# Optimization experiments

Hardware: AMD Instinct MI355X
Metric: run time of the kernel (lower is better)

Reference implementation:

```python
import jax, jax.numpy as jnp
import numpy as np

D_MODEL = 320
N_CH = 129
N_TIMES = 200
D_STATE = 32
HEADDIM = 32
D_CONV = 4
N_LAYERS = 4
N_HEADS = 16
EPS = 1e-5


def _ln(x, w, b):
    m = jnp.mean(x, -1, keepdims=True)
    v = jnp.var(x, -1, keepdims=True)
    return (x - m) / jnp.sqrt(v + EPS) * w + b


def _mha(x, wqkv, bqkv, wo, bo, h):
    # torch nn.MultiheadAttention (batch_first, eval mode, avg attn weights)
    B, L, D = x.shape
    hd = D // h
    qkv = x @ wqkv.T + bqkv
    q, k, v = jnp.split(qkv, 3, axis=-1)
    sp = lambda t: t.reshape(B, L, h, hd).transpose(0, 2, 1, 3)
    q, k, v = sp(q), sp(k), sp(v)
    attn = jax.nn.softmax(jnp.einsum('bhqd,bhkd->bhqk', q, k) / np.sqrt(hd).astype(np.float32), axis=-1)
    o = jnp.einsum('bhqk,bhkd->bhqd', attn, v).transpose(0, 2, 1, 3).reshape(B, L, D)
    return o @ wo.T + bo, attn.mean(axis=1)


def _mamba2(u, in_w, conv_w, conv_b, dt_bias, A_log, Dskip, gn_w, out_w):
    # Mamba2 block, reference (non-fused) path, ngroups=1
    B, L, D = u.shape
    din = 2 * D
    H = din // HEADDIM
    P, N = HEADDIM, D_STATE
    zxbcdt = u @ in_w.T                       # (B,L,2*din+2N+H)
    z = zxbcdt[..., :din]
    xBC = zxbcdt[..., din:2 * din + 2 * N]
    dt = jax.nn.softplus(zxbcdt[..., -H:] + dt_bias)   # (B,L,H)
    # causal depthwise conv1d, kernel D_CONV, then silu
    xp = jnp.pad(xBC, ((0, 0), (D_CONV - 1, 0), (0, 0)))
    xc = conv_b + sum(xp[:, k:k + L, :] * conv_w[:, k] for k in range(D_CONV))
    xc = xc * jax.nn.sigmoid(xc)
    xh = xc[..., :din].reshape(B, L, H, P)
    Bm = xc[..., din:din + N]                 # (B,L,N)
    Cm = xc[..., din + N:]                    # (B,L,N)
    dA = jnp.exp(dt * (-jnp.exp(A_log)))      # (B,L,H)

    def step(st, inp):
        dA_t, dt_t, x_t, B_t, C_t = inp
        st = st * dA_t[:, :, None, None] + jnp.einsum('bh,bhp,bn->bhpn', dt_t, x_t, B_t)
        return st, jnp.einsum('bhpn,bn->bhp', st, C_t)

    mv = lambda t: jnp.moveaxis(t, 1, 0)
    st0 = jnp.zeros((B, H, P, N), u.dtype)
    _, ys = jax.lax.scan(step, st0, (mv(dA), mv(dt), mv(xh), mv(Bm), mv(Cm)))
    y = jnp.moveaxis(ys, 0, 1) + Dskip[None, None, :, None] * xh   # (B,L,H,P)
    y = y.reshape(B, L, din) * (z * jax.nn.sigmoid(z))             # gate
    y = y * jax.lax.rsqrt(jnp.mean(y * y, -1, keepdims=True) + EPS) * gn_w
    return y @ out_w.T


def _forward(x, sp_conv_w, sp_conv_b, sp_qkv_w, sp_qkv_b, sp_out_w, sp_out_b,
             sp_ln1_w, sp_ln1_b, sp_ff1_w, sp_ff1_b, sp_ff2_w, sp_ff2_b,
             sp_ln2_w, sp_ln2_b, norm_in_w, norm_in_b,
             m_in_w, m_conv_w, m_conv_b, m_dt_bias, m_A_log, m_D, m_gnorm_w, m_out_w,
             ln_w, ln_b, pm_qkv_w, pm_qkv_b, pm_out_w, pm_out_b, pm_ln_w, pm_ln_b,
             pool_w1, pool_b1, pool_w2, pool_b2, head_w1, head_b1, head_w2, head_b2):
    # spatial encoder: 1x1 conv projection -> MHA -> FFN
    h = jnp.einsum('bcl,dc->bld', x, sp_conv_w) + sp_conv_b        # (B,L,D)
    ha, sp_attn = _mha(h, sp_qkv_w, sp_qkv_b, sp_out_w, sp_out_b, N_HEADS)
    h = _ln(h + ha, sp_ln1_w, sp_ln1_b)
    ff = jax.nn.gelu(h @ sp_ff1_w.T + sp_ff1_b, approximate=False) @ sp_ff2_w.T + sp_ff2_b
    h = _ln(h + ff, sp_ln2_w, sp_ln2_b)
    h = _ln(h, norm_in_w, norm_in_b)
    # stacked pre-norm Mamba2 blocks with residuals
    for i in range(N_LAYERS):
        res = h
        h = _ln(h, ln_w[i], ln_b[i])
        h = _mamba2(h, m_in_w[i], m_conv_w[i], m_conv_b[i], m_dt_bias[i],
                    m_A_log[i], m_D[i], m_gnorm_w[i], m_out_w[i])
        h = h + res
    ha, post_attn = _mha(h, pm_qkv_w, pm_qkv_b, pm_out_w, pm_out_b, N_HEADS)
    h = _ln(h + ha, pm_ln_w, pm_ln_b)
    # attention-weighted pooling
    a = jnp.tanh(h @ pool_w1.T + pool_b1) @ pool_w2.T + pool_b2    # (B,L,1)
    a = jax.nn.softmax(a, axis=1)
    pooled = jnp.sum(h * a, axis=1)                                # (B,D)
    hr = jax.nn.gelu(pooled @ head_w1.T + head_b1, approximate=False)
    out = hr @ head_w2.T + head_b2                                 # (B,1)
    return out, sp_attn, post_attn, a.squeeze(-1)


def setup_inputs() -> dict:
    key = jax.random.key(0)
    ks = iter(jax.random.split(key, 64))
    nrm = lambda shape, s=0.02: jax.random.normal(next(ks), shape, jnp.float32) * s
    d, C, L, B = D_MODEL, N_CH, N_TIMES, 128
    din = 2 * d
    Hm = din // HEADDIM                       # 20 SSM heads
    dproj = 2 * din + 2 * D_STATE + Hm        # 1364
    cdim = din + 2 * D_STATE                  # 704
    nl = N_LAYERS
    return {
        'x': jax.random.normal(next(ks), (B, C, L), jnp.float32),
        'sp_conv_w': nrm((d, C)), 'sp_conv_b': jnp.zeros((d,), jnp.float32),
        'sp_qkv_w': nrm((3 * d, d)), 'sp_qkv_b': jnp.zeros((3 * d,), jnp.float32),
        'sp_out_w': nrm((d, d)), 'sp_out_b': jnp.zeros((d,), jnp.float32),
        'sp_ln1_w': jnp.ones((d,), jnp.float32), 'sp_ln1_b': jnp.zeros((d,), jnp.float32),
        'sp_ff1_w': nrm((2 * d, d)), 'sp_ff1_b': jnp.zeros((2 * d,), jnp.float32),
        'sp_ff2_w': nrm((d, 2 * d)), 'sp_ff2_b': jnp.zeros((d,), jnp.float32),
        'sp_ln2_w': jnp.ones((d,), jnp.float32), 'sp_ln2_b': jnp.zeros((d,), jnp.float32),
        'norm_in_w': jnp.ones((d,), jnp.float32), 'norm_in_b': jnp.zeros((d,), jnp.float32),
        'm_in_w': nrm((nl, dproj, d)),
        'm_conv_w': nrm((nl, cdim, D_CONV), 0.2),
        'm_conv_b': jnp.zeros((nl, cdim), jnp.float32),
        'm_dt_bias': jax.random.uniform(next(ks), (nl, Hm), jnp.float32, -0.1, 0.1),
        'm_A_log': jnp.log(jax.random.uniform(next(ks), (nl, Hm), jnp.float32, 1.0, 16.0)),
        'm_D': jnp.ones((nl, Hm), jnp.float32),
        'm_gnorm_w': jnp.ones((nl, din), jnp.float32),
        'm_out_w': nrm((nl, d, din)),
        'ln_w': jnp.ones((nl, d), jnp.float32), 'ln_b': jnp.zeros((nl, d), jnp.float32),
        'pm_qkv_w': nrm((3 * d, d)), 'pm_qkv_b': jnp.zeros((3 * d,), jnp.float32),
        'pm_out_w': nrm((d, d)), 'pm_out_b': jnp.zeros((d,), jnp.float32),
        'pm_ln_w': jnp.ones((d,), jnp.float32), 'pm_ln_b': jnp.zeros((d,), jnp.float32),
        'pool_w1': nrm((d // 4, d)), 'pool_b1': jnp.zeros((d // 4,), jnp.float32),
        'pool_w2': nrm((1, d // 4)), 'pool_b2': jnp.zeros((1,), jnp.float32),
        'head_w1': nrm((d // 2, d)), 'head_b1': jnp.zeros((d // 2,), jnp.float32),
        'head_w2': nrm((1, d // 2)), 'head_b2': jnp.zeros((1,), jnp.float32),
    }


def reference(x, sp_conv_w, sp_conv_b, sp_qkv_w, sp_qkv_b, sp_out_w, sp_out_b,
              sp_ln1_w, sp_ln1_b, sp_ff1_w, sp_ff1_b, sp_ff2_w, sp_ff2_b,
              sp_ln2_w, sp_ln2_b, norm_in_w, norm_in_b,
              m_in_w, m_conv_w, m_conv_b, m_dt_bias, m_A_log, m_D, m_gnorm_w, m_out_w,
              ln_w, ln_b, pm_qkv_w, pm_qkv_b, pm_out_w, pm_out_b, pm_ln_w, pm_ln_b,
              pool_w1, pool_b1, pool_w2, pool_b2, head_w1, head_b1, head_w2, head_b2):
    return _forward(x, sp_conv_w, sp_conv_b, sp_qkv_w, sp_qkv_b, sp_out_w, sp_out_b,
                    sp_ln1_w, sp_ln1_b, sp_ff1_w, sp_ff1_b, sp_ff2_w, sp_ff2_b,
                    sp_ln2_w, sp_ln2_b, norm_in_w, norm_in_b,
                    m_in_w, m_conv_w, m_conv_b, m_dt_bias, m_A_log, m_D, m_gnorm_w, m_out_w,
                    ln_w, ln_b, pm_qkv_w, pm_qkv_b, pm_out_w, pm_out_b, pm_ln_w, pm_ln_b,
                    pool_w1, pool_b1, pool_w2, pool_b2, head_w1, head_b1, head_w2, head_b2)
```

## Files before the change

kernel.cpp:

```cpp
#include <hip/hip_runtime.h>
#include <math.h>

#define BB 128
#define LL 200
#define DM 320
#define RTOT (BB*LL)
#define NCH 129
#define DIN 640
#define HM 20
#define PP 32
#define NN 32
#define CDIM 704
#define DPROJ 1364
#define NH 16
#define HD 20
#define ATTN_SCALE 0.22360679774997896f

#define CH 32
#define NCHUNK 4
#define RC (CH*LL)

static __device__ __forceinline__ float sigmoidf_(float x){ return 1.f/(1.f+__expf(-x)); }
static __device__ __forceinline__ float geluf_(float x){ return 0.5f*x*(1.f+erff(x*0.70710678118654752f)); }

__global__ __launch_bounds__(256) void k_transpose(const float* __restrict__ x, float* __restrict__ xT){
  int idx = blockIdx.x*256 + threadIdx.x;
  if (idx >= BB*LL*NCH) return;
  int r = idx / NCH, c = idx - r*NCH;
  int b = r / LL, l = r - b*LL;
  xT[idx] = x[((size_t)b*NCH + c)*LL + l];
}

#define BM 128
#define BN 64
#define BKK 16
__global__ __launch_bounds__(256) void k_gemm(const float* __restrict__ A, const float* __restrict__ W,
    const float* __restrict__ bias, float* __restrict__ C, int M, int N, int K, int act, int accum){
  __shared__ float As[BKK][BM+4];
  __shared__ float Ws[BKK][BN+4];
  int tid = threadIdx.x;
  int m0 = blockIdx.y*BM, n0 = blockIdx.x*BN;
  int tx = tid & 15, ty = tid >> 4;
  float acc[8][4];
  #pragma unroll
  for (int i=0;i<8;i++)
    #pragma unroll
    for (int j=0;j<4;j++) acc[i][j]=0.f;
  bool kvec = ((K & 3) == 0);
  for (int k0 = 0; k0 < K; k0 += BKK) {
    if (kvec) {
      int r = tid >> 2, c4 = (tid & 3) << 2;
      #pragma unroll
      for (int hfl = 0; hfl < 2; hfl++) {
        int rr = r + hfl*64;
        float4 v = make_float4(0.f,0.f,0.f,0.f);
        if (m0 + rr < M && k0 + c4 < K)
          v = *(const float4*)(A + (size_t)(m0+rr)*K + k0 + c4);
        As[c4+0][rr]=v.x; As[c4+1][rr]=v.y; As[c4+2][rr]=v.z; As[c4+3][rr]=v.w;
      }
      {
        int n = tid >> 2;
        float4 v = make_float4(0.f,0.f,0.f,0.f);
        if (n0 + n < N && k0 + c4 < K)
          v = *(const float4*)(W + (size_t)(n0+n)*K + k0 + c4);
        Ws[c4+0][n]=v.x; Ws[c4+1][n]=v.y; Ws[c4+2][n]=v.z; Ws[c4+3][n]=v.w;
      }
    } else {
      #pragma unroll
      for (int e = 0; e < 8; e++) {
        int lin = e*256 + tid;
        int r = lin >> 4, c = lin & 15;
        float v = 0.f;
        if (m0 + r < M && k0 + c < K) v = A[(size_t)(m0+r)*K + k0 + c];
        As[c][r] = v;
      }
      #pragma unroll
      for (int e = 0; e < 4; e++) {
        int lin = e*256 + tid;
        int n = lin >> 4, c = lin & 15;
        float v = 0.f;
        if (n0 + n < N && k0 + c < K) v = W[(size_t)(n0+n)*K + k0 + c];
        Ws[c][n] = v;
      }
    }
    __syncthreads();
    #pragma unroll
    for (int kk = 0; kk < BKK; kk++) {
      float af[8], bf[4];
      float4 a0 = *(const float4*)&As[kk][ty*8];
      float4 a1 = *(const float4*)&As[kk][ty*8+4];
      af[0]=a0.x; af[1]=a0.y; af[2]=a0.z; af[3]=a0.w;
      af[4]=a1.x; af[5]=a1.y; af[6]=a1.z; af[7]=a1.w;
      float4 b0 = *(const float4*)&Ws[kk][tx*4];
      bf[0]=b0.x; bf[1]=b0.y; bf[2]=b0.z; bf[3]=b0.w;
      #pragma unroll
      for (int i=0;i<8;i++)
        #pragma unroll
        for (int j=0;j<4;j++) acc[i][j] = fmaf(af[i], bf[j], acc[i][j]);
// ... 7 lines not shown
    #pragma unroll
    for (int j=0;j<4;j++){
      int n = n0 + tx*4 + j;
      if (n >= N) continue;
      float v = acc[i][j];
      if (bias) v += bias[n];
      if (act == 1) v = geluf_(v);
      else if (act == 2) v = tanhf(v);
      size_t off = (size_t)m*N + n;
      if (accum) v += C[off];
      C[off] = v;
    }
  }
}

__global__ __launch_bounds__(256) void k_ln(const float* __restrict__ A, const float* __restrict__ Badd,
    float* __restrict__ O, const float* __restrict__ w, const float* __restrict__ b, int nrows){
  int wid = threadIdx.x >> 6, lane = threadIdx.x & 63;
  int row = blockIdx.x*4 + wid;
  if (row >= nrows) return;
  const float* a = A + (size_t)row*DM;
  float x[5]; float s = 0.f;
  #pragma unroll
  for (int j=0;j<5;j++){
    int c = lane + j*64;
    x[j] = a[c];
    if (Badd) x[j] += Badd[(size_t)row*DM + c];
    s += x[j];
  }
  #pragma unroll
  for (int m=1;m<64;m<<=1) s += __shfl_xor(s, m);
  float mean = s * (1.f/DM);
  float vs = 0.f;
  #pragma unroll
  for (int j=0;j<5;j++){ float d = x[j]-mean; vs += d*d; }
  #pragma unroll
  for (int m=1;m<64;m<<=1) vs += __shfl_xor(vs, m);
  float inv = rsqrtf(vs*(1.f/DM) + 1e-5f);
  float* o = O + (size_t)row*DM;
  #pragma unroll
  for (int j=0;j<5;j++){
    int c = lane + j*64;
    o[c] = (x[j]-mean)*inv*w[c] + b[c];
  }
}

__global__ __launch_bounds__(256) void k_attn1(const float* __restrict__ qkv,
    float* __restrict__ oout, float* __restrict__ ml){
  __shared__ float Ks[LL*HD];
  __shared__ float Vs[LL*HD];
  int b = blockIdx.x >> 4, h = blockIdx.x & 15;
  int tid = threadIdx.x;
  for (int idx = tid; idx < LL*HD; idx += 256) {
    int r = idx / HD, c = idx - r*HD;
    const float* base = qkv + (size_t)(b*LL+r)*960 + h*HD + c;
    Ks[idx] = base[320];
    Vs[idx] = base[640];
  }
  __syncthreads();
  int q = tid;
  if (q >= LL) return;
  const float* qp = qkv + (size_t)(b*LL+q)*960 + h*HD;
  float qr[HD];
// ... 8 lines not shown
  for (int d=0; d<HD; d++) o[d]=0.f;
  for (int k = 0; k < LL; k++) {
    float s = 0.f;
    #pragma unroll
    for (int d = 0; d < HD; d++) s = fmaf(qr[d], Ks[k*HD+d], s);
    s *= ATTN_SCALE;
    float nm = fmaxf(m, s);
    float al = __expf(m - nm);
    float p  = __expf(s - nm);
    l = l*al + p;
    #pragma unroll
    for (int d = 0; d < HD; d++) o[d] = fmaf(p, Vs[k*HD+d], o[d]*al);
    m = nm;
  }
  float inv = 1.f/l;
  float* op = oout + (size_t)(b*LL+q)*DM + h*HD;
  #pragma unroll
  for (int d = 0; d < HD; d++) op[d] = o[d]*inv;
  size_t mlb = ((size_t)(b*NH+h)*LL + q)*2;
  ml[mlb+0] = m;
  ml[mlb+1] = l;
}

#define QS 164
__global__ __launch_bounds__(256) void k_attnmean(const float* __restrict__ qkv,
    const float* __restrict__ ml, float* __restrict__ outp){
  __shared__ float Qs[32*QS];
  __shared__ float Ksh[32*QS];
  __shared__ float Ms[NH*32];
  __shared__ float Ls[NH*32];
  int b = blockIdx.z;
  int q0 = blockIdx.y*32, k0 = blockIdx.x*32;
  int tid = threadIdx.x;
// ... 37 lines not shown
          float4 v = *(const float4*)&Qs[qr*QS + hh*HD + d4*4];
          s += v.x*kf[d4*4] + v.y*kf[d4*4+1] + v.z*kf[d4*4+2] + v.w*kf[d4*4+3];
        }
        acc[j] += __expf(s*ATTN_SCALE - Ms[h*32 + qr]) * Ls[h*32 + qr];
      }
    }
  }
  #pragma unroll
  for (int j = 0; j < 4; j++) {
    int q = q0 + ty + j*8, k = k0 + tx;
    if (q < LL && k < LL)
      outp[(size_t)(b*LL+q)*LL + k] = acc[j] * (1.f/NH);
  }
}

__global__ __launch_bounds__(256) void k_dtdA(const float* __restrict__ big, const float* __restrict__ dtb,
    const float* __restrict__ alog, float* __restrict__ dt, float* __restrict__ da, int nrows){
  int idx = blockIdx.x*256 + threadIdx.x;
  if (idx >= nrows*HM) return;
  int row = idx / HM, h = idx - row*HM;
  float raw = big[(size_t)row*DPROJ + 1344 + h] + dtb[h];
  float sp = (raw > 30.f) ? raw : log1pf(__expf(raw));
  dt[idx] = sp;
  da[idx] = __expf(-__expf(alog[h]) * sp);
}

__global__ __launch_bounds__(256) void k_conv(const float* __restrict__ big, const float* __restrict__ cw,
    const float* __restrict__ cb, float* __restrict__ xc, int nrows){
  int idx = blockIdx.x*256 + threadIdx.x;
  if (idx >= nrows*CDIM) return;
  int row = idx / CDIM, c = idx - row*CDIM;
  int l = row % LL;
  float acc = cb[c];
  #pragma unroll
  for (int k = 0; k < 4; k++) {
    int li = l - 3 + k;
    if (li >= 0) acc = fmaf(big[(size_t)(row-3+k)*DPROJ + 640 + c], cw[c*4+k], acc);
  }
  xc[idx] = acc * sigmoidf_(acc);
}

__global__ __launch_bounds__(256) void k_scan(const float* __restrict__ xc, const float* __restrict__ dt,
    const float* __restrict__ da, float* __restrict__ y){
  __shared__ float xs[LL*PP];
  __shared__ float dts[LL];
  __shared__ float das[LL];
  int b = blockIdx.x / HM, h = blockIdx.x - (blockIdx.x/HM)*HM;
  int tid = threadIdx.x;
  for (int idx = tid; idx < LL*PP; idx += 256) {
    int r = idx >> 5, c = idx & 31;
    xs[idx] = xc[(size_t)(b*LL+r)*CDIM + h*PP + c];
  }
  for (int idx = tid; idx < LL; idx += 256) {
    dts[idx] = dt[(b*LL+idx)*HM + h];
    das[idx] = da[(b*LL+idx)*HM + h];
  }
  __syncthreads();
  int p = tid >> 3, ng = tid & 7, n0 = ng*4;
  float st0=0.f, st1=0.f, st2=0.f, st3=0.f;
  const float* base = xc + (size_t)(b*LL)*CDIM;
  float4 Bc = *(const float4*)(base + 640 + n0);
  float4 Cc = *(const float4*)(base + 672 + n0);
  for (int t = 0; t < LL; t++) {
    float4 Bn = Bc, Cn = Cc;
    if (t < LL-1) {
      Bn = *(const float4*)(base + (size_t)(t+1)*CDIM + 640 + n0);
      Cn = *(const float4*)(base + (size_t)(t+1)*CDIM + 672 + n0);
    }
    float dav = das[t], dtv = dts[t];
    float coef = dtv * xs[t*PP + p];
    st0 = fmaf(coef, Bc.x, st0*dav);
    st1 = fmaf(coef, Bc.y, st1*dav);
    st2 = fmaf(coef, Bc.z, st2*dav);
    st3 = fmaf(coef, Bc.w, st3*dav);
    float part = st0*Cc.x + st1*Cc.y + st2*Cc.z + st3*Cc.w;
    part += __shfl_xor(part, 1);
    part += __shfl_xor(part, 2);
    part += __shfl_xor(part, 4);
    if (ng == 0) y[(size_t)(b*LL+t)*DIN + h*PP + p] = part;
    Bc = Bn; Cc = Cn;
  }
}

__global__ __launch_bounds__(256) void k_mpost(float* __restrict__ y, const float* __restrict__ xc,
    const float* __restrict__ zbuf, const float* __restrict__ Dp, const float* __restrict__ gw, int nrows){
  int wid = threadIdx.x >> 6, lane = threadIdx.x & 63;
  int row = blockIdx.x*4 + wid;
  if (row >= nrows) return;
  float v[10]; float ss = 0.f;
  #pragma unroll
  for (int j = 0; j < 10; j++) {
    int c = lane + j*64;
    float ys = y[(size_t)row*DIN + c];
    float xh = xc[(size_t)row*CDIM + c];
    float z  = zbuf[(size_t)row*DPROJ + c];
    float val = (ys + Dp[c>>5]*xh) * (z * sigmoidf_(z));
    v[j] = val; ss += val*val;
  }
  #pragma unroll
  for (int m=1;m<64;m<<=1) ss += __shfl_xor(ss, m);
  float scale = rsqrtf(ss*(1.f/DIN) + 1e-5f);
  #pragma unroll
  for (int j = 0; j < 10; j++) {
    int c = lane + j*64;
    y[(size_t)row*DIN + c] = v[j]*scale*gw[c];
  }
}

__global__ __launch_bounds__(256) void k_pool2(const float* __restrict__ A, const float* __restrict__ w2,
    const float* __restrict__ b2, float* __restrict__ out, int nrows){
  int row = blockIdx.x*256 + threadIdx.x;
  if (row >= nrows) return;
  float s = b2[0];
  const float* a = A + (size_t)row*80;
  #pragma unroll
  for (int j = 0; j < 80; j++) s = fmaf(a[j], w2[j], s);
  out[row] = s;
}

__global__ __launch_bounds__(256) void k_pool(const float* __restrict__ logits, const float* __restrict__ h,
// ... 17 lines not shown
    pooled[b*DM + d] = s;
  }
}

__global__ __launch_bounds__(128) void k_head2(const float* __restrict__ hr, const float* __restrict__ w2,
    const float* __restrict__ b2, float* __restrict__ out){
  int b = threadIdx.x;
  if (b >= BB) return;
  float s = b2[0];
  const float* a = hr + (size_t)b*160;
  #pragma unroll
  for (int j = 0; j < 160; j++) s = fmaf(a[j], w2[j], s);
  out[b] = s;
}

static inline void gemm_launch(const float* A, const float* W, const float* bias, float* C,
    int M, int N, int K, int act, int accum, hipStream_t s){
  dim3 g((N+BN-1)/BN, (M+BM-1)/BM);
  hipLaunchKernelGGL(k_gemm, g, dim3(256), 0, s, A, W, bias, C, M, N, K, act, accum);
}

#define F_H    ((size_t)0)
#define F_T    ((size_t)8192000)
#define F_S    ((size_t)16384000)
#define F_BIGC ((size_t)16384000)
#define F_XCC  ((size_t)25113600)
#define F_YC   ((size_t)29619200)
#define F_DTC  ((size_t)33715200)
#define F_DAC  ((size_t)33843200)
#define F_QKVC ((size_t)16384000)
#define F_MLC  ((size_t)22528000)
#define F_DEST ((size_t)22732800)
#define F_FF1  ((size_t)16384000)
#define F_XT   ((size_t)16384000)
#define F_P1   ((size_t)16384000)
#define F_LOG  ((size_t)18432000)
#define F_PL   ((size_t)18457600)
#define F_HR   ((size_t)18498560)

#define O_OUT ((size_t)0)
#define O_A1  ((size_t)128)
#define O_A2  ((size_t)5120128)
#define O_A   ((size_t)10240128)

extern "C" void kernel_launch(void* const* d_in, const int* in_sizes, int n_in,
                              void* d_out, int out_size, void* d_ws, size_t ws_size,
                              hipStream_t stream) {
  const float* x         = (const float*)d_in[0];
  const float* sp_conv_w = (const float*)d_in[1];
  const float* sp_conv_b = (const float*)d_in[2];
  const float* sp_qkv_w  = (const float*)d_in[3];
  const float* sp_qkv_b  = (const float*)d_in[4];
  const float* sp_out_w  = (const float*)d_in[5];
// ... 23 lines not shown
  const float* pm_out_w  = (const float*)d_in[29];
  const float* pm_out_b  = (const float*)d_in[30];
  const float* pm_ln_w   = (const float*)d_in[31];
  const float* pm_ln_b   = (const float*)d_in[32];
  const float* pool_w1   = (const float*)d_in[33];
  const float* pool_b1   = (const float*)d_in[34];
  const float* pool_w2   = (const float*)d_in[35];
  const float* pool_b2   = (const float*)d_in[36];
  const float* head_w1   = (const float*)d_in[37];
  const float* head_b1   = (const float*)d_in[38];
  const float* head_w2   = (const float*)d_in[39];
  const float* head_b2   = (const float*)d_in[40];

  float* ws  = (float*)d_ws;
  float* H   = ws + F_H;
  float* T   = ws + F_T;
  float* out = (float*)d_out;

  hipLaunchKernelGGL(k_transpose, dim3((BB*LL*NCH+255)/256), dim3(256), 0, stream, x, ws + F_XT);
  gemm_launch(ws + F_XT, sp_conv_w, sp_conv_b, H, RTOT, DM, NCH, 0, 0, stream);

  for (int c = 0; c < NCHUNK; c++) {
    const float* Hc = H + (size_t)c*RC*DM;
    gemm_launch(Hc, sp_qkv_w, sp_qkv_b, ws + F_QKVC, RC, 3*DM, DM, 0, 0, stream);
    hipLaunchKernelGGL(k_attn1, dim3(CH*NH), dim3(256), 0, stream, ws + F_QKVC,
                       T + (size_t)c*RC*DM, ws + F_MLC);
    hipLaunchKernelGGL(k_attnmean, dim3(7,7,CH), dim3(256), 0, stream, ws + F_QKVC,
                       ws + F_MLC, out + O_A1 + (size_t)c*RC*LL);
  }
  gemm_launch(T, sp_out_w, sp_out_b, ws + F_DEST, RTOT, DM, DM, 0, 0, stream);
  hipLaunchKernelGGL(k_ln, dim3(RTOT/4), dim3(256), 0, stream, H, ws + F_DEST, H, sp_ln1_w, sp_ln1_b, RTOT);

  gemm_launch(H, sp_ff1_w, sp_ff1_b, ws + F_FF1, RTOT, DIN, DM, 1, 0, stream);
  gemm_launch(ws + F_FF1, sp_ff2_w, sp_ff2_b, T, RTOT, DM, DIN, 0, 0, stream);
  hipLaunchKernelGGL(k_ln, dim3(RTOT/4), dim3(256), 0, stream, H, T, H, sp_ln2_w, sp_ln2_b, RTOT);
  hipLaunchKernelGGL(k_ln, dim3(RTOT/4), dim3(256), 0, stream, H, (const float*)nullptr, H, norm_in_w, norm_in_b, RTOT);

  for (int i = 0; i < 4; i++) {
    hipLaunchKernelGGL(k_ln, dim3(RTOT/4), dim3(256), 0, stream, H, (const float*)nullptr, T,
                       ln_w + (size_t)i*DM, ln_b + (size_t)i*DM, RTOT);
    for (int c = 0; c < NCHUNK; c++) {
      const float* Tc = T + (size_t)c*RC*DM;
      float* BIGc = ws + F_BIGC;
      float* XCc  = ws + F_XCC;
      float* Yc   = ws + F_YC;
      float* DTc  = ws + F_DTC;
      float* DAc  = ws + F_DAC;
      gemm_launch(Tc, m_in_w + (size_t)i*DPROJ*DM, nullptr, BIGc, RC, DPROJ, DM, 0, 0, stream);
      hipLaunchKernelGGL(k_dtdA, dim3((RC*HM+255)/256), dim3(256), 0, stream, BIGc,
                         m_dt_bias + (size_t)i*HM, m_A_log + (size_t)i*HM, DTc, DAc, RC);
      hipLaunchKernelGGL(k_conv, dim3((RC*CDIM+255)/256), dim3(256), 0, stream, BIGc,
                         m_conv_w + (size_t)i*CDIM*4, m_conv_b + (size_t)i*CDIM, XCc, RC);
      hipLaunchKernelGGL(k_scan, dim3(CH*HM), dim3(256), 0, stream, XCc, DTc, DAc, Yc);
      hipLaunchKernelGGL(k_mpost, dim3(RC/4), dim3(256), 0, stream, Yc, XCc, BIGc,
                         m_D + (size_t)i*HM, m_gnorm_w + (size_t)i*DIN, RC);
      gemm_launch(Yc, m_out_w + (size_t)i*DM*DIN, nullptr, H + (size_t)c*RC*DM, RC, DM, DIN, 0, 1, stream);
    }
  }

  for (int c = 0; c < NCHUNK; c++) {
    const float* Hc = H + (size_t)c*RC*DM;
    gemm_launch(Hc, pm_qkv_w, pm_qkv_b, ws + F_QKVC, RC, 3*DM, DM, 0, 0, stream);
    hipLaunchKernelGGL(k_attn1, dim3(CH*NH), dim3(256), 0, stream, ws + F_QKVC,
                       T + (size_t)c*RC*DM, ws + F_MLC);
    hipLaunchKernelGGL(k_attnmean, dim3(7,7,CH), dim3(256), 0, stream, ws + F_QKVC,
                       ws + F_MLC, out + O_A2 + (size_t)c*RC*LL);
  }
  gemm_launch(T, pm_out_w, pm_out_b, ws + F_DEST, RTOT, DM, DM, 0, 0, stream);
  hipLaunchKernelGGL(k_ln, dim3(RTOT/4), dim3(256), 0, stream, H, ws + F_DEST, H, pm_ln_w, pm_ln_b, RTOT);

  gemm_launch(H, pool_w1, pool_b1, ws + F_P1, RTOT, 80, DM, 2, 0, stream);
  hipLaunchKernelGGL(k_pool2, dim3((RTOT+255)/256), dim3(256), 0, stream, ws + F_P1, pool_w2, pool_b2, ws + F_LOG, RTOT);
  hipLaunchKernelGGL(k_pool, dim3(BB), dim3(256), 0, stream, ws + F_LOG, H, out + O_A, ws + F_PL);
  gemm_launch(ws + F_PL, head_w1, head_b1, ws + F_HR, BB, 160, DM, 1, 0, stream);
  hipLaunchKernelGGL(k_head2, dim3(1), dim3(128), 0, stream, ws + F_HR, head_w2, head_b2, out + O_OUT);
}
```

Before: 7.652 ms.

## Replace FP32 SIMT GEMMs with split-bf16 MFMA GEMMs and restructure chunked pipeline

Swaps the scalar FP32 tiled GEMM for an MFMA bf16 kernel. Each FP32 operand is split into three bf16 parts (hi/mid/lo) and six cross products are accumulated to keep near-FP32 accuracy. Producers (LN, attention, mpost, transpose) now emit the split bf16 triples directly, and weights are split on every call. It also fuses the double LayerNorm, folds dt/dA into the scan, and re-chunks the spatial and Mamba stages. The aim is to use matrix cores for the GEMM-bound work, at the cost of six MFMAs per product, extra split traffic and per-call weight-splitting kernels.

```diff
diff --git a/kernel.cpp b/kernel.cpp
--- a/kernel.cpp
+++ b/kernel.cpp
@@ -15,20 +15,123 @@
 #define NH 16
 #define HD 20
 #define ATTN_SCALE 0.22360679774997896f
+#define KCONV 160
 
 #define CH 32
 #define NCHUNK 4
 #define RC (CH*LL)
+#define CHB 16
+#define NCHUNKB 8
+#define RCB (CHB*LL)
+
+typedef unsigned short ushort;
+typedef __attribute__((ext_vector_type(8))) short v8s;
+typedef __attribute__((ext_vector_type(4))) float v4f;
 
 static __device__ __forceinline__ float sigmoidf_(float x){ return 1.f/(1.f+__expf(-x)); }
 static __device__ __forceinline__ float geluf_(float x){ return 0.5f*x*(1.f+erff(x*0.70710678118654752f)); }
-
-__global__ __launch_bounds__(256) void k_transpose(const float* __restrict__ x, float* __restrict__ xT){
-  int idx = blockIdx.x*256 + threadIdx.x;
-  if (idx >= BB*LL*NCH) return;
-  int r = idx / NCH, c = idx - r*NCH;
-  int b = r / LL, l = r - b*LL;
-  xT[idx] = x[((size_t)b*NCH + c)*LL + l];
+static __device__ __forceinline__ ushort f2bf(float f){
+  unsigned u = __float_as_uint(f);
+  u = (u + 0x7FFFu + ((u>>16)&1u)) >> 16;
+  return (ushort)u;
+}
+static __device__ __forceinline__ float bf2f(ushort h){ return __uint_as_float(((unsigned)h)<<16); }
+static __device__ __forceinline__ void split3(float v, ushort* h, ushort* m, ushort* l){
+  ushort hh = f2bf(v);
+  float r1 = v - bf2f(hh);
+  ushort mm = f2bf(r1);
+  float r2 = r1 - bf2f(mm);
+  *h = hh; *m = mm; *l = f2bf(r2);
+}
+
+__global__ __launch_bounds__(256) void k_mgemm(
+    const ushort* __restrict__ AH, const ushort* __restrict__ AM, const ushort* __restrict__ AL,
+    const ushort* __restrict__ WH, const ushort* __restrict__ WM, const ushort* __restrict__ WL,
+    const float* __restrict__ bias,
+    float* __restrict__ outF, ushort* __restrict__ outH, ushort* __restrict__ outM, ushort* __restrict__ outL,
+    int M, int N, int K, int act, int accum){
+  __shared__ ushort sA[3][128*32];
+  __shared__ ushort sW[3][128*32];
+  int tid = threadIdx.x;
+  int wid = tid>>6, lane = tid&63;
+  int quad = lane>>4, col = lane&15;
+  int m0 = blockIdx.y*128, n0 = blockIdx.x*128;
+  int wm = (wid&1)*64, wn = (wid>>1)*64;
+  v4f acc[4][4];
+  #pragma unroll
+  for (int i=0;i<4;i++)
+    #pragma unroll
+    for (int j=0;j<4;j++) acc[i][j] = (v4f)(0.f);
+
+  int r0 = tid>>2, kc0 = (tid&3)<<3;
+  int r1 = r0 + 64, kc1 = kc0;
+  int wrow0 = n0+r0; if (wrow0 > N-1) wrow0 = N-1;
+  int wrow1 = n0+r1; if (wrow1 > N-1) wrow1 = N-1;
+  const ushort* pA[3] = {AH, AM, AL};
+  const ushort* pW[3] = {WH, WM, WL};
+  size_t aoff0 = (size_t)(m0+r0)*K + kc0;
+  size_t aoff1 = (size_t)(m0+r1)*K + kc1;
+  size_t woff0 = (size_t)wrow0*K + kc0;
+  size_t woff1 = (size_t)wrow1*K + kc1;
+  int so0 = r0*32 + kc0, so1 = r1*32 + kc1;
+
+  for (int kb = 0; kb < K; kb += 32) {
+    #pragma unroll
+    for (int s=0;s<3;s++){
+      v8s va0 = *(const v8s*)(pA[s]+aoff0+kb);
+      v8s va1 = *(const v8s*)(pA[s]+aoff1+kb);
+      v8s vw0 = *(const v8s*)(pW[s]+woff0+kb);
+      v8s vw1 = *(const v8s*)(pW[s]+woff1+kb);
+      *(v8s*)&sA[s][so0]=va0; *(v8s*)&sA[s][so1]=va1;
+      *(v8s*)&sW[s][so0]=vw0; *(v8s*)&sW[s][so1]=vw1;
+    }
+    __syncthreads();
+    v8s af[3][4];
+    #pragma unroll
+    for (int i=0;i<4;i++){
+      int ro = (wm+16*i+col)*32 + quad*8;
+      af[0][i] = *(const v8s*)&sA[0][ro];
+      af[1][i] = *(const v8s*)&sA[1][ro];
+      af[2][i] = *(const v8s*)&sA[2][ro];
+    }
+    #pragma unroll
+    for (int j=0;j<4;j++){
+      int ro = (wn+16*j+col)*32 + quad*8;
+      v8s b0 = *(const v8s*)&sW[0][ro];
+      v8s b1 = *(const v8s*)&sW[1][ro];
+      v8s b2 = *(const v8s*)&sW[2][ro];
+      #pragma unroll
+      for (int i=0;i<4;i++){
+        acc[i][j] = __builtin_amdgcn_mfma_f32_16x16x32_bf16(af[2][i], b0, acc[i][j], 0,0,0);
+        acc[i][j] = __builtin_amdgcn_mfma_f32_16x16x32_bf16(af[1][i], b1, acc[i][j], 0,0,0);
+        acc[i][j] = __builtin_amdgcn_mfma_f32_16x16x32_bf16(af[0][i], b2, acc[i][j], 0,0,0);
+        acc[i][j] = __builtin_amdgcn_mfma_f32_16x16x32_bf16(af[1][i], b0, acc[i][j], 0,0,0);
+        acc[i][j] = __builtin_amdgcn_mfma_f32_16x16x32_bf16(af[0][i], b1, acc[i][j], 0,0,0);
+        acc[i][j] = __builtin_amdgcn_mfma_f32_16x16x32_bf16(af[0][i], b0, acc[i][j], 0,0,0);
+      }
+    }
+    __syncthreads();
+  }
+  #pragma unroll
+  for (int i=0;i<4;i++){
+    int mb = m0 + wm + 16*i + quad*4;
+    #pragma unroll
+    for (int j=0;j<4;j++){
+      int n = n0 + wn + 16*j + col;
+      if (n >= N) continue;
+      float bv = bias ? bias[n] : 0.f;
+      #pragma unroll
+      for (int r=0;r<4;r++){
+        float v = acc[i][j][r] + bv;
+        if (act == 1) v = geluf_(v);
+        else if (act == 2) v = tanhf(v);
+        size_t off = (size_t)(mb+r)*N + n;
+        if (accum) v += outF[off];
+        if (outF) outF[off] = v;
+        if (outH) split3(v, outH+off, outM+off, outL+off);
+      }
+    }
+  }
 }
 
 #define BM 128
@@ -46,42 +149,22 @@
   for (int i=0;i<8;i++)
     #pragma unroll
     for (int j=0;j<4;j++) acc[i][j]=0.f;
-  bool kvec = ((K & 3) == 0);
   for (int k0 = 0; k0 < K; k0 += BKK) {
-    if (kvec) {
-      int r = tid >> 2, c4 = (tid & 3) << 2;
-      #pragma unroll
-      for (int hfl = 0; hfl < 2; hfl++) {
-        int rr = r + hfl*64;
-        float4 v = make_float4(0.f,0.f,0.f,0.f);
-        if (m0 + rr < M && k0 + c4 < K)
-          v = *(const float4*)(A + (size_t)(m0+rr)*K + k0 + c4);
-        As[c4+0][rr]=v.x; As[c4+1][rr]=v.y; As[c4+2][rr]=v.z; As[c4+3][rr]=v.w;
-      }
-      {
-        int n = tid >> 2;
-        float4 v = make_float4(0.f,0.f,0.f,0.f);
-        if (n0 + n < N && k0 + c4 < K)
-          v = *(const float4*)(W + (size_t)(n0+n)*K + k0 + c4);
-        Ws[c4+0][n]=v.x; Ws[c4+1][n]=v.y; Ws[c4+2][n]=v.z; Ws[c4+3][n]=v.w;
-      }
-    } else {
-      #pragma unroll
-      for (int e = 0; e < 8; e++) {
-        int lin = e*256 + tid;
-        int r = lin >> 4, c = lin & 15;
-        float v = 0.f;
-        if (m0 + r < M && k0 + c < K) v = A[(size_t)(m0+r)*K + k0 + c];
-        As[c][r] = v;
-      }
-      #pragma unroll
-      for (int e = 0; e < 4; e++) {
-        int lin = e*256 + tid;
-        int n = lin >> 4, c = lin & 15;
-        float v = 0.f;
-        if (n0 + n < N && k0 + c < K) v = W[(size_t)(n0+n)*K + k0 + c];
-        Ws[c][n] = v;
-      }
+    int r = tid >> 2, c4 = (tid & 3) << 2;
+    #pragma unroll
+    for (int hfl = 0; hfl < 2; hfl++) {
+      int rr = r + hfl*64;
+      float4 v = make_float4(0.f,0.f,0.f,0.f);
+      if (m0 + rr < M && k0 + c4 < K)
+        v = *(const float4*)(A + (size_t)(m0+rr)*K + k0 + c4);
+      As[c4+0][rr]=v.x; As[c4+1][rr]=v.y; As[c4+2][rr]=v.z; As[c4+3][rr]=v.w;
+    }
+    {
+      int n = tid >> 2;
+      float4 v = make_float4(0.f,0.f,0.f,0.f);
+      if (n0 + n < N && k0 + c4 < K)
+        v = *(const float4*)(W + (size_t)(n0+n)*K + k0 + c4);
+      Ws[c4+0][n]=v.x; Ws[c4+1][n]=v.y; Ws[c4+2][n]=v.z; Ws[c4+3][n]=v.w;
     }
     __syncthreads();
     #pragma unroll
@@ -119,8 +202,36 @@
   }
 }
 
+__global__ __launch_bounds__(256) void k_wsplit(const float* __restrict__ src, ushort* __restrict__ hi,
+    ushort* __restrict__ mi, ushort* __restrict__ lo, int N, int K, int Kp){
+  int idx = blockIdx.x*256 + threadIdx.x;
+  if (idx >= N*Kp) return;
+  int n = idx / Kp, k = idx - n*Kp;
+  float v = (k < K) ? src[(size_t)n*K + k] : 0.f;
+  split3(v, hi+idx, mi+idx, lo+idx);
+}
+
+__global__ __launch_bounds__(256) void k_split(const float* __restrict__ src, ushort* __restrict__ hi,
+    ushort* __restrict__ mi, ushort* __restrict__ lo, int n){
+  int idx = blockIdx.x*256 + threadIdx.x;
+  if (idx >= n) return;
+  split3(src[idx], hi+idx, mi+idx, lo+idx);
+}
+
+__global__ __launch_bounds__(256) void k_tsplit(const float* __restrict__ x, ushort* __restrict__ hi,
+    ushort* __restrict__ mi, ushort* __restrict__ lo, int r0g){
+  int idx = blockIdx.x*256 + threadIdx.x;
+  if (idx >= RC*KCONV) return;
+  int r = idx / KCONV, c = idx - r*KCONV;
+  int gr = r0g + r;
+  int b = gr / LL, l = gr - b*LL;
+  float v = (c < NCH) ? x[((size_t)b*NCH + c)*LL + l] : 0.f;
+  split3(v, hi+idx, mi+idx, lo+idx);
+}
+
 __global__ __launch_bounds__(256) void k_ln(const float* __restrict__ A, const float* __restrict__ Badd,
-    float* __restrict__ O, const float* __restrict__ w, const float* __restrict__ b, int nrows){
+    float* __restrict__ Of, ushort* __restrict__ Oh, ushort* __restrict__ Om, ushort* __restrict__ Ol,
+    const float* __restrict__ w, const float* __restrict__ b, int nrows){
   int wid = threadIdx.x >> 6, lane = threadIdx.x & 63;
   int row = blockIdx.x*4 + wid;
   if (row >= nrows) return;
@@ -142,16 +253,64 @@
   #pragma unroll
   for (int m=1;m<64;m<<=1) vs += __shfl_xor(vs, m);
   float inv = rsqrtf(vs*(1.f/DM) + 1e-5f);
-  float* o = O + (size_t)row*DM;
   #pragma unroll
   for (int j=0;j<5;j++){
     int c = lane + j*64;
-    o[c] = (x[j]-mean)*inv*w[c] + b[c];
+    float v = (x[j]-mean)*inv*w[c] + b[c];
+    size_t off = (size_t)row*DM + c;
+    if (Of) Of[off] = v;
+    if (Oh) split3(v, Oh+off, Om+off, Ol+off);
+  }
+}
+
+__global__ __launch_bounds__(256) void k_ln2x(const float* __restrict__ A, const float* __restrict__ F,
+    const float* __restrict__ w2, const float* __restrict__ b2,
+    const float* __restrict__ w3, const float* __restrict__ b3,
+    float* __restrict__ O, int nrows){
+  int wid = threadIdx.x >> 6, lane = threadIdx.x & 63;
+  int row = blockIdx.x*4 + wid;
+  if (row >= nrows) return;
+  float x[5]; float s = 0.f;
+  #pragma unroll
+  for (int j=0;j<5;j++){
+    int c = lane + j*64;
+    x[j] = A[(size_t)row*DM + c] + F[(size_t)row*DM + c];
+    s += x[j];
+  }
+  #pragma unroll
+  for (int m=1;m<64;m<<=1) s += __shfl_xor(s, m);
+  float mean = s * (1.f/DM);
+  float vs = 0.f;
+  #pragma unroll
+  for (int j=0;j<5;j++){ float d = x[j]-mean; vs += d*d; }
+  #pragma unroll
+  for (int m=1;m<64;m<<=1) vs += __shfl_xor(vs, m);
+  float inv = rsqrtf(vs*(1.f/DM) + 1e-5f);
+  float s2 = 0.f;
+  #pragma unroll
+  for (int j=0;j<5;j++){
+    int c = lane + j*64;
+    x[j] = (x[j]-mean)*inv*w2[c] + b2[c];
+    s2 += x[j];
+  }
+  #pragma unroll
+  for (int m=1;m<64;m<<=1) s2 += __shfl_xor(s2, m);
+  float mean2 = s2 * (1.f/DM);
+  float vs2 = 0.f;
+  #pragma unroll
+  for (int j=0;j<5;j++){ float d = x[j]-mean2; vs2 += d*d; }
+  #pragma unroll
+  for (int m=1;m<64;m<<=1) vs2 += __shfl_xor(vs2, m);
+  float inv2 = rsqrtf(vs2*(1.f/DM) + 1e-5f);
+  #pragma unroll
+  for (int j=0;j<5;j++){
+    int c = lane + j*64;
+    O[(size_t)row*DM + c] = (x[j]-mean2)*inv2*w3[c] + b3[c];
   }
 }
 
 __global__ __launch_bounds__(256) void k_attn1(const float* __restrict__ qkv,
-    float* __restrict__ oout, float* __restrict__ ml){
+    ushort* __restrict__ oh, ushort* __restrict__ om, ushort* __restrict__ ol, float* __restrict__ ml){
   __shared__ float Ks[LL*HD];
   __shared__ float Vs[LL*HD];
   int b = blockIdx.x >> 4, h = blockIdx.x & 15;
@@ -190,9 +349,11 @@
     m = nm;
   }
   float inv = 1.f/l;
-  float* op = oout + (size_t)(b*LL+q)*DM + h*HD;
-  #pragma unroll
-  for (int d = 0; d < HD; d++) op[d] = o[d]*inv;
+  size_t ob = (size_t)(b*LL+q)*DM + h*HD;
+  #pragma unroll
+  for (int d = 0; d < HD; d++) {
+    split3(o[d]*inv, oh+ob+d, om+ob+d, ol+ob+d);
+  }
   size_t mlb = ((size_t)(b*NH+h)*LL + q)*2;
   ml[mlb+0] = m;
   ml[mlb+1] = l;
@@ -260,17 +421,6 @@
   }
 }
 
-__global__ __launch_bounds__(256) void k_dtdA(const float* __restrict__ big, const float* __restrict__ dtb,
-    const float* __restrict__ alog, float* __restrict__ dt, float* __restrict__ da, int nrows){
-  int idx = blockIdx.x*256 + threadIdx.x;
-  if (idx >= nrows*HM) return;
-  int row = idx / HM, h = idx - row*HM;
-  float raw = big[(size_t)row*DPROJ + 1344 + h] + dtb[h];
-  float sp = (raw > 30.f) ? raw : log1pf(__expf(raw));
-  dt[idx] = sp;
-  da[idx] = __expf(-__expf(alog[h]) * sp);
-}
-
 __global__ __launch_bounds__(256) void k_conv(const float* __restrict__ big, const float* __restrict__ cw,
     const float* __restrict__ cb, float* __restrict__ xc, int nrows){
   int idx = blockIdx.x*256 + threadIdx.x;
@@ -286,8 +436,8 @@
   xc[idx] = acc * sigmoidf_(acc);
 }
 
-__global__ __launch_bounds__(256) void k_scan(const float* __restrict__ xc, const float* __restrict__ dt,
-    const float* __restrict__ da, float* __restrict__ y){
+__global__ __launch_bounds__(256) void k_scan(const float* __restrict__ xc, const float* __restrict__ big,
+    const float* __restrict__ dtb, const float* __restrict__ alog, float* __restrict__ y){
   __shared__ float xs[LL*PP];
   __shared__ float dts[LL];
   __shared__ float das[LL];
@@ -297,9 +447,13 @@
     int r = idx >> 5, c = idx & 31;
     xs[idx] = xc[(size_t)(b*LL+r)*CDIM + h*PP + c];
   }
+  float aexp = __expf(alog[h]);
+  float dtbh = dtb[h];
   for (int idx = tid; idx < LL; idx += 256) {
-    dts[idx] = dt[(b*LL+idx)*HM + h];
-    das[idx] = da[(b*LL+idx)*HM + h];
+    float raw = big[(size_t)(b*LL+idx)*DPROJ + 1344 + h] + dtbh;
+    float sp = (raw > 30.f) ? raw : log1pf(__expf(raw));
+    dts[idx] = sp;
+    das[idx] = __expf(-aexp * sp);
   }
   __syncthreads();
   int p = tid >> 3, ng = tid & 7, n0 = ng*4;
@@ -328,8 +482,9 @@
   }
 }
 
-__global__ __launch_bounds__(256) void k_mpost(float* __restrict__ y, const float* __restrict__ xc,
-    const float* __restrict__ zbuf, const float* __restrict__ Dp, const float* __restrict__ gw, int nrows){
+__global__ __launch_bounds__(256) void k_mpost(const float* __restrict__ y, const float* __restrict__ xc,
+    const float* __restrict__ zbuf, const float* __restrict__ Dp, const float* __restrict__ gw,
+    ushort* __restrict__ yh, ushort* __restrict__ ym, ushort* __restrict__ yl, int nrows){
   int wid = threadIdx.x >> 6, lane = threadIdx.x & 63;
   int row = blockIdx.x*4 + wid;
   if (row >= nrows) return;
@@ -349,7 +504,9 @@
   #pragma unroll
   for (int j = 0; j < 10; j++) {
     int c = lane + j*64;
-    y[(size_t)row*DIN + c] = v[j]*scale*gw[c];
+    float val = v[j]*scale*gw[c];
+    size_t off = (size_t)row*DIN + c;
+    split3(val, yh+off, ym+off, yl+off);
   }
 }
 
@@ -397,29 +554,77 @@
   out[b] = s;
 }
 
-static inline void gemm_launch(const float* A, const float* W, const float* bias, float* C,
+static inline void mgemm(const ushort* AH, const ushort* AM, const ushort* AL,
+    const ushort* WH, const ushort* WM, const ushort* WL,
+    const float* bias, float* outF, ushort* outH, ushort* outM, ushort* outL,
     int M, int N, int K, int act, int accum, hipStream_t s){
-  dim3 g((N+BN-1)/BN, (M+BM-1)/BM);
-  hipLaunchKernelGGL(k_gemm, g, dim3(256), 0, s, A, W, bias, C, M, N, K, act, accum);
-}
-
-#define F_H    ((size_t)0)
-#define F_T    ((size_t)8192000)
-#define F_S    ((size_t)16384000)
-#define F_BIGC ((size_t)16384000)
-#define F_XCC  ((size_t)25113600)
-#define F_YC   ((size_t)29619200)
-#define F_DTC  ((size_t)33715200)
-#define F_DAC  ((size_t)33843200)
-#define F_QKVC ((size_t)16384000)
-#define F_MLC  ((size_t)22528000)
-#define F_DEST ((size_t)22732800)
-#define F_FF1  ((size_t)16384000)
-#define F_XT   ((size_t)16384000)
-#define F_P1   ((size_t)16384000)
-#define F_LOG  ((size_t)18432000)
-#define F_PL   ((size_t)18457600)
-#define F_HR   ((size_t)18498560)
+  hipLaunchKernelGGL(k_mgemm, dim3((N+127)/128, M/128), dim3(256), 0, s,
+                     AH, AM, AL, WH, WM, WL, bias, outF, outH, outM, outL, M, N, K, act, accum);
+}
+static inline void wsplit(const float* src, ushort* hi, ushort* mi, ushort* lo, int N, int K, int Kp, hipStream_t s){
+  hipLaunchKernelGGL(k_wsplit, dim3((N*Kp+255)/256), dim3(256), 0, s, src, hi, mi, lo, N, K, Kp);
+}
+
+#define F_H      ((size_t)0)
+#define F_WCONVH ((size_t)8192000)
+#define F_WCONVM ((size_t)8217600)
+#define F_WCONVL ((size_t)8243200)
+#define F_WQKVH  ((size_t)8268800)
+#define F_WQKVM  ((size_t)8422400)
+#define F_WQKVL  ((size_t)8576000)
+#define F_WOUTH  ((size_t)8729600)
+#define F_WOUTM  ((size_t)8780800)
+#define F_WOUTL  ((size_t)8832000)
+#define F_WFF1H  ((size_t)8883200)
+#define F_WFF1M  ((size_t)8985600)
+#define F_WFF1L  ((size_t)9088000)
+#define F_WFF2H  ((size_t)9190400)
+#define F_WFF2M  ((size_t)9292800)
+#define F_WFF2L  ((size_t)9395200)
+#define F_WINH   ((size_t)9497600)
+#define F_WINM   ((size_t)10370560)
+#define F_WINL   ((size_t)11243520)
+#define F_WMOH   ((size_t)12116480)
+#define F_WMOM   ((size_t)12526080)
+#define F_WMOL   ((size_t)12935680)
+#define F_WPQH   ((size_t)13345280)
+#define F_WPQM   ((size_t)13498880)
+#define F_WPQL   ((size_t)13652480)
+#define F_WPOH   ((size_t)13806080)
+#define F_WPOM   ((size_t)13857280)
+#define F_WPOL   ((size_t)13908480)
+#define F_WPLH   ((size_t)13959680)
+#define F_WPLM   ((size_t)13972480)
+#define F_WPLL   ((size_t)13985280)
+#define SB       ((size_t)13998080)
+#define S_XTH  (SB+0)
+#define S_XTM  (SB+512000)
+#define S_XTL  (SB+1024000)
+#define S_HH   (SB+1536000)
+#define S_HM   (SB+2560000)
+#define S_HL   (SB+3584000)
+#define S_TH   (SB+4608000)
+#define S_TM   (SB+5632000)
+#define S_TL   (SB+6656000)
+#define S_QKV  (SB+7680000)
+#define S_FF1H (SB+7680000)
+#define S_FF1M (SB+9728000)
+#define S_FF1L (SB+11776000)
+#define S_P1   (SB+7680000)
+#define S_ML   (SB+13824000)
+#define S_DEST (SB+14028800)
+#define S_LOG  (SB+16076800)
+#define S_PL   (SB+16102400)
+#define S_HR   (SB+16143360)
+#define S_MTH  (SB+0)
+#define S_MTM  (SB+512000)
+#define S_MTL  (SB+1024000)
+#define S_BIG  (SB+1536000)
+#define S_XC   (SB+5900800)
+#define S_YC   (SB+8153600)
+#define S_YH   (SB+10201600)
+#define S_YM   (SB+11225600)
+#define S_YL   (SB+12249600)
 
 #define O_OUT ((size_t)0)
 #define O_A1  ((size_t)128)
@@ -473,64 +678,97 @@
 
   float* ws  = (float*)d_ws;
   float* H   = ws + F_H;
-  float* T   = ws + F_T;
   float* out = (float*)d_out;
 
-  hipLaunchKernelGGL(k_transpose, dim3((BB*LL*NCH+255)/256), dim3(256), 0, stream, x, ws + F_XT);
-  gemm_launch(ws + F_XT, sp_conv_w, sp_conv_b, H, RTOT, DM, NCH, 0, 0, stream);
+  #define U(off) ((ushort*)(ws + (off)))
+
+  wsplit(sp_conv_w, U(F_WCONVH), U(F_WCONVM), U(F_WCONVL), DM, NCH, KCONV, stream);
+  wsplit(sp_qkv_w,  U(F_WQKVH),  U(F_WQKVM),  U(F_WQKVL),  3*DM, DM, DM, stream);
+  wsplit(sp_out_w,  U(F_WOUTH),  U(F_WOUTM),  U(F_WOUTL),  DM, DM, DM, stream);
+  wsplit(sp_ff1_w,  U(F_WFF1H),  U(F_WFF1M),  U(F_WFF1L),  DIN, DM, DM, stream);
+  wsplit(sp_ff2_w,  U(F_WFF2H),  U(F_WFF2M),  U(F_WFF2L),  DM, DIN, DIN, stream);
+  for (int i = 0; i < 4; i++) {
+    size_t wo = (size_t)i*DPROJ*DM;
+    wsplit(m_in_w + wo, U(F_WINH)+wo, U(F_WINM)+wo, U(F_WINL)+wo, DPROJ, DM, DM, stream);
+    size_t wo2 = (size_t)i*DM*DIN;
+    wsplit(m_out_w + wo2, U(F_WMOH)+wo2, U(F_WMOM)+wo2, U(F_WMOL)+wo2, DM, DIN, DIN, stream);
+  }
+  wsplit(pm_qkv_w, U(F_WPQH), U(F_WPQM), U(F_WPQL), 3*DM, DM, DM, stream);
+  wsplit(pm_out_w, U(F_WPOH), U(F_WPOM), U(F_WPOL), DM, DM, DM, stream);
+  wsplit(pool_w1,  U(F_WPLH), U(F_WPLM), U(F_WPLL), 80, DM, DM, stream);
 
   for (int c = 0; c < NCHUNK; c++) {
-    const float* Hc = H + (size_t)c*RC*DM;
-    gemm_launch(Hc, sp_qkv_w, sp_qkv_b, ws + F_QKVC, RC, 3*DM, DM, 0, 0, stream);
-    hipLaunchKernelGGL(k_attn1, dim3(CH*NH), dim3(256), 0, stream, ws + F_QKVC,
-                       T + (size_t)c*RC*DM, ws + F_MLC);
-    hipLaunchKernelGGL(k_attnmean, dim3(7,7,CH), dim3(256), 0, stream, ws + F_QKVC,
-                       ws + F_MLC, out + O_A1 + (size_t)c*RC*LL);
-  }
-  gemm_launch(T, sp_out_w, sp_out_b, ws + F_DEST, RTOT, DM, DM, 0, 0, stream);
-  hipLaunchKernelGGL(k_ln, dim3(RTOT/4), dim3(256), 0, stream, H, ws + F_DEST, H, sp_ln1_w, sp_ln1_b, RTOT);
-
-  gemm_launch(H, sp_ff1_w, sp_ff1_b, ws + F_FF1, RTOT, DIN, DM, 1, 0, stream);
-  gemm_launch(ws + F_FF1, sp_ff2_w, sp_ff2_b, T, RTOT, DM, DIN, 0, 0, stream);
-  hipLaunchKernelGGL(k_ln, dim3(RTOT/4), dim3(256), 0, stream, H, T, H, sp_ln2_w, sp_ln2_b, RTOT);
-  hipLaunchKernelGGL(k_ln, dim3(RTOT/4), dim3(256), 0, stream, H, (const float*)nullptr, H, norm_in_w, norm_in_b, RTOT);
+    float* Hc = H + (size_t)c*RC*DM;
+    hipLaunchKernelGGL(k_tsplit, dim3((RC*KCONV+255)/256), dim3(256), 0, stream, x,
+                       U(S_XTH), U(S_XTM), U(S_XTL), c*RC);
+    mgemm(U(S_XTH), U(S_XTM), U(S_XTL), U(F_WCONVH), U(F_WCONVM), U(F_WCONVL), sp_conv_b,
+          Hc, U(S_HH), U(S_HM), U(S_HL), RC, DM, KCONV, 0, 0, stream);
+    mgemm(U(S_HH), U(S_HM), U(S_HL), U(F_WQKVH), U(F_WQKVM), U(F_WQKVL), sp_qkv_b,
+          ws + S_QKV, nullptr, nullptr, nullptr, RC, 3*DM, DM, 0, 0, stream);
+    hipLaunchKernelGGL(k_attn1, dim3(CH*NH), dim3(256), 0, stream, ws + S_QKV,
+                       U(S_TH), U(S_TM), U(S_TL), ws + S_ML);
+    hipLaunchKernelGGL(k_attnmean, dim3(7,7,CH), dim3(256), 0, stream, ws + S_QKV,
+                       ws + S_ML, out + O_A1 + (size_t)c*RC*LL);
+    mgemm(U(S_TH), U(S_TM), U(S_TL), U(F_WOUTH), U(F_WOUTM), U(F_WOUTL), sp_out_b,
+          ws + S_DEST, nullptr, nullptr, nullptr, RC, DM, DM, 0, 0, stream);
+    hipLaunchKernelGGL(k_ln, dim3(RC/4), dim3(256), 0, stream, Hc, ws + S_DEST,
+                       Hc, U(S_HH), U(S_HM), U(S_HL), sp_ln1_w, sp_ln1_b, RC);
+    mgemm(U(S_HH), U(S_HM), U(S_HL), U(F_WFF1H), U(F_WFF1M), U(F_WFF1L), sp_ff1_b,
+          nullptr, U(S_FF1H), U(S_FF1M), U(S_FF1L), RC, DIN, DM, 1, 0, stream);
+    mgemm(U(S_FF1H), U(S_FF1M), U(S_FF1L), U(F_WFF2H), U(F_WFF2M), U(F_WFF2L), sp_ff2_b,
+          ws + S_DEST, nullptr, nullptr, nullptr, RC, DM, DIN, 0, 0, stream);
+    hipLaunchKernelGGL(k_ln2x, dim3(RC/4), dim3(256), 0, stream, Hc, ws + S_DEST,
+                       sp_ln2_w, sp_ln2_b, norm_in_w, norm_in_b, Hc, RC);
+  }
 
   for (int i = 0; i < 4; i++) {
-    hipLaunchKernelGGL(k_ln, dim3(RTOT/4), dim3(256), 0, stream, H, (const float*)nullptr, T,
-                       ln_w + (size_t)i*DM, ln_b + (size_t)i*DM, RTOT);
-    for (int c = 0; c < NCHUNK; c++) {
-      const float* Tc = T + (size_t)c*RC*DM;
-      float* BIGc = ws + F_BIGC;
-      float* XCc  = ws + F_XCC;
-      float* Yc   = ws + F_YC;
-      float* DTc  = ws + F_DTC;
-      float* DAc  = ws + F_DAC;
-      gemm_launch(Tc, m_in_w + (size_t)i*DPROJ*DM, nullptr, BIGc, RC, DPROJ, DM, 0, 0, stream);
-      hipLaunchKernelGGL(k_dtdA, dim3((RC*HM+255)/256), dim3(256), 0, stream, BIGc,
-                         m_dt_bias + (size_t)i*HM, m_A_log + (size_t)i*HM, DTc, DAc, RC);
-      hipLaunchKernelGGL(k_conv, dim3((RC*CDIM+255)/256), dim3(256), 0, stream, BIGc,
-                         m_conv_w + (size_t)i*CDIM*4, m_conv_b + (size_t)i*CDIM, XCc, RC);
-      hipLaunchKernelGGL(k_scan, dim3(CH*HM), dim3(256), 0, stream, XCc, DTc, DAc, Yc);
-      hipLaunchKernelGGL(k_mpost, dim3(RC/4), dim3(256), 0, stream, Yc, XCc, BIGc,
-                         m_D + (size_t)i*HM, m_gnorm_w + (size_t)i*DIN, RC);
-      gemm_launch(Yc, m_out_w + (size_t)i*DM*DIN, nullptr, H + (size_t)c*RC*DM, RC, DM, DIN, 0, 1, stream);
+    const ushort* WIH = U(F_WINH) + (size_t)i*DPROJ*DM;
+    const ushort* WIM = U(F_WINM) + (size_t)i*DPROJ*DM;
+    const ushort* WIL = U(F_WINL) + (size_t)i*DPROJ*DM;
+    const ushort* WOH = U(F_WMOH) + (size_t)i*DM*DIN;
+    const ushort* WOM = U(F_WMOM) + (size_t)i*DM*DIN;
+    const ushort* WOL = U(F_WMOL) + (size_t)i*DM*DIN;
+    for (int c = 0; c < NCHUNKB; c++) {
+      float* Hc = H + (size_t)c*RCB*DM;
+      hipLaunchKernelGGL(k_ln, dim3(RCB/4), dim3(256), 0, stream, Hc, (const float*)nullptr,
+                         (float*)nullptr, U(S_MTH), U(S_MTM), U(S_MTL),
+                         ln_w + (size_t)i*DM, ln_b + (size_t)i*DM, RCB);
+      mgemm(U(S_MTH), U(S_MTM), U(S_MTL), WIH, WIM, WIL, nullptr,
+            ws + S_BIG, nullptr, nullptr, nullptr, RCB, DPROJ, DM, 0, 0, stream);
+      hipLaunchKernelGGL(k_conv, dim3((RCB*CDIM+255)/256), dim3(256), 0, stream, ws + S_BIG,
+                         m_conv_w + (size_t)i*CDIM*4, m_conv_b + (size_t)i*CDIM, ws + S_XC, RCB);
+      hipLaunchKernelGGL(k_scan, dim3(CHB*HM), dim3(256), 0, stream, ws + S_XC, ws + S_BIG,
+                         m_dt_bias + (size_t)i*HM, m_A_log + (size_t)i*HM, ws + S_YC);
+      hipLaunchKernelGGL(k_mpost, dim3(RCB/4), dim3(256), 0, stream, ws + S_YC, ws + S_XC, ws + S_BIG,
+                         m_D + (size_t)i*HM, m_gnorm_w + (size_t)i*DIN,
+                         U(S_YH), U(S_YM), U(S_YL), RCB);
+      mgemm(U(S_YH), U(S_YM), U(S_YL), WOH, WOM, WOL, nullptr,
+            Hc, nullptr, nullptr, nullptr, RCB, DM, DIN, 0, 1, stream);
     }
   }
 
   for (int c = 0; c < NCHUNK; c++) {
-    const float* Hc = H + (size_t)c*RC*DM;
-    gemm_launch(Hc, pm_qkv_w, pm_qkv_b, ws + F_QKVC, RC, 3*DM, DM, 0, 0, stream);
-    hipLaunchKernelGGL(k_attn1, dim3(CH*NH), dim3(256), 0, stream, ws + F_QKVC,
-                       T + (size_t)c*RC*DM, ws + F_MLC);
-    hipLaunchKernelGGL(k_attnmean, dim3(7,7,CH), dim3(256), 0, stream, ws + F_QKVC,
-                       ws + F_MLC, out + O_A2 + (size_t)c*RC*LL);
-  }
-  gemm_launch(T, pm_out_w, pm_out_b, ws + F_DEST, RTOT, DM, DM, 0, 0, stream);
-  hipLaunchKernelGGL(k_ln, dim3(RTOT/4), dim3(256), 0, stream, H, ws + F_DEST, H, pm_ln_w, pm_ln_b, RTOT);
-
-  gemm_launch(H, pool_w1, pool_b1, ws + F_P1, RTOT, 80, DM, 2, 0, stream);
-  hipLaunchKernelGGL(k_pool2, dim3((RTOT+255)/256), dim3(256), 0, stream, ws + F_P1, pool_w2, pool_b2, ws + F_LOG, RTOT);
-  hipLaunchKernelGGL(k_pool, dim3(BB), dim3(256), 0, stream, ws + F_LOG, H, out + O_A, ws + F_PL);
-  gemm_launch(ws + F_PL, head_w1, head_b1, ws + F_HR, BB, 160, DM, 1, 0, stream);
-  hipLaunchKernelGGL(k_head2, dim3(1), dim3(128), 0, stream, ws + F_HR, head_w2, head_b2, out + O_OUT);
-}
+    float* Hc = H + (size_t)c*RC*DM;
+    hipLaunchKernelGGL(k_split, dim3((RC*DM+255)/256), dim3(256), 0, stream, Hc,
+                       U(S_HH), U(S_HM), U(S_HL), RC*DM);
+    mgemm(U(S_HH), U(S_HM), U(S_HL), U(F_WPQH), U(F_WPQM), U(F_WPQL), pm_qkv_b,
+          ws + S_QKV, nullptr, nullptr, nullptr, RC, 3*DM, DM, 0, 0, stream);
+    hipLaunchKernelGGL(k_attn1, dim3(CH*NH), dim3(256), 0, stream, ws + S_QKV,
+                       U(S_TH), U(S_TM), U(S_TL), ws + S_ML);
+    hipLaunchKernelGGL(k_attnmean, dim3(7,7,CH), dim3(256), 0, stream, ws + S_QKV,
+                       ws + S_ML, out + O_A2 + (size_t)c*RC*LL);
+    mgemm(U(S_TH), U(S_TM), U(S_TL), U(F_WPOH), U(F_WPOM), U(F_WPOL), pm_out_b,
+          ws + S_DEST, nullptr, nullptr, nullptr, RC, DM, DM, 0, 0, stream);
+    hipLaunchKernelGGL(k_ln, dim3(RC/4), dim3(256), 0, stream, Hc, ws + S_DEST,
+                       Hc, U(S_HH), U(S_HM), U(S_HL), pm_ln_w, pm_ln_b, RC);
+    mgemm(U(S_HH), U(S_HM), U(S_HL), U(F_WPLH), U(F_WPLM), U(F_WPLL), pool_b1,
+          ws + S_P1, nullptr, nullptr, nullptr, RC, 80, DM, 2, 0, stream);
+    hipLaunchKernelGGL(k_pool2, dim3((RC+255)/256), dim3(256), 0, stream, ws + S_P1, pool_w2, pool_b2,
+                       ws + S_LOG + (size_t)c*RC, RC);
+  }
+
+  hipLaunchKernelGGL(k_pool, dim3(BB), dim3(256), 0, stream, ws + S_LOG, H, out + O_A, ws + S_PL);
+  hipLaunchKernelGGL(k_gemm, dim3((160+BN-1)/BN, (BB+BM-1)/BM), dim3(256), 0, stream,
+                     ws + S_PL, head_w1, head_b1, ws + S_HR, BB, 160, DM, 1, 0);
+  hipLaunchKernelGGL(k_head2, dim3(1), dim3(128), 0, stream, ws + S_HR, head_w2, head_b2, out + O_OUT);
+}
```

Result: slower. 9.569 ms (+25.1%).
